# Optimization experiments

Hardware: AMD Instinct MI355X
Metric: run time of the kernel (lower is better)

## Reference

```python
import jax, jax.numpy as jnp
import numpy as np

NEG_SLOPE = 0.3

def capped_lrelu(x):
    # clamp(LeakyReLU_0.3(x), max=1)
    return jnp.minimum(jnp.where(x >= 0, x, NEG_SLOPE * x), 1.0)

def setup_inputs() -> dict:
    key = jax.random.key(0)
    ks = jax.random.split(key, 8)
    B, T, V, H, O = 64, 512, 512, 256, 512
    s = 1.0 / np.sqrt(H)
    return {
        "sentence": jax.random.normal(ks[0], (B, T, V), dtype=jnp.float32),
        "prev_state": jnp.zeros((1, B, H), dtype=jnp.float32),
        "W_ih": jax.random.normal(ks[1], (H, V), dtype=jnp.float32) * s,
        "b_ih": jax.random.normal(ks[2], (H,), dtype=jnp.float32) * s,
        "W_hh": jax.random.normal(ks[3], (H, H), dtype=jnp.float32) * s,
        "b_hh": jax.random.normal(ks[4], (H,), dtype=jnp.float32) * s,
        "W_out": jax.random.normal(ks[5], (O, H), dtype=jnp.float32) * s,
        "b_out": jax.random.normal(ks[6], (O,), dtype=jnp.float32) * s,
    }

def reference(sentence, prev_state, W_ih, b_ih, W_hh, b_hh, W_out, b_out):
    # nn.RNN(nonlinearity='relu'), batch_first, n_layers=1:
    #   h_t = relu(x_t @ W_ih^T + b_ih + h_{t-1} @ W_hh^T + b_hh)
    # Precompute input projections for all timesteps, scan the recurrence.
    x_proj = jnp.einsum('btv,hv->bth', sentence, W_ih) + b_ih  # [B,T,H]
    x_proj_t = jnp.swapaxes(x_proj, 0, 1)                      # [T,B,H]
    h0 = prev_state[0]                                         # [B,H]

    def step(h, xt):
        h_new = jax.nn.relu(xt + h @ W_hh.T + b_hh)
        return h_new, h_new

    h_last, out_seq = jax.lax.scan(step, h0, x_proj_t)         # [T,B,H]
    out_seq = jnp.swapaxes(out_seq, 0, 1)                      # [B,T,H]

    hidden_activ = capped_lrelu(out_seq)
    tags = jax.nn.sigmoid(jnp.einsum('bth,oh->bto', hidden_activ, W_out) + b_out)
    h_n = h_last[None]                                         # [1,B,H]
    return tags, h_n
```

## Files before the change

kernel.cpp:

```cpp
#include <hip/hip_runtime.h>
#include <hip/hip_bf16.h>


typedef __attribute__((ext_vector_type(8))) _Float16 half8;
typedef __attribute__((ext_vector_type(4))) _Float16 half4;
typedef __attribute__((ext_vector_type(4))) float   floatx4;

__device__ __forceinline__ void lds_barrier() {
    asm volatile("s_waitcnt lgkmcnt(0)\n\ts_barrier" ::: "memory");
}

__global__ void conv_weights(const float* __restrict__ wih, const float* __restrict__ wout,
                             _Float16* __restrict__ out) {
    int idx = blockIdx.x * blockDim.x + threadIdx.x;
    const float* src = (idx < 32768) ? wih : wout;
    int j = idx & 32767;
    float4 v = ((const float4*)src)[j];
    half4 h = { (_Float16)v.x, (_Float16)v.y, (_Float16)v.z, (_Float16)v.w };
    ((half4*)out)[idx] = h;
}

__device__ __forceinline__ void stage_weights_swz(const _Float16* __restrict__ src,
                                                  int rowStrideHalves,
                                                  _Float16* lds) {
    int wave = threadIdx.x >> 6;
    int lane = threadIdx.x & 63;
#pragma unroll
    for (int j = 0; j < 16; j++) {
        int Lb = j * 8192 + wave * 1024 + lane * 16;
        int n  = Lb >> 9;
        int c  = Lb & 511;
        int cs = c ^ ((n & 7) << 4);
        const _Float16* g = src + (size_t)n * rowStrideHalves + (cs >> 1);
        _Float16* l = lds + (j * 8192 + wave * 1024) / 2;
        __builtin_amdgcn_global_load_lds((const __attribute__((address_space(1))) void*)g,
                                         (__attribute__((address_space(3))) void*)l,
                                         16, 0, 0);
    }
    asm volatile("s_waitcnt vmcnt(0)" ::: "memory");
    __syncthreads();
}

__global__ __launch_bounds__(512, 2) void gemm1_xproj(const float* __restrict__ A,
                                                      const _Float16* __restrict__ Bw,
                                                      const float* __restrict__ b_ih,
                                                      const float* __restrict__ b_hh,
                                                      float* __restrict__ C) {
    const int K = 512, N = 256;
    __shared__ _Float16 ldsB[65536];
    int wave = threadIdx.x >> 6;
    int lane = threadIdx.x & 63;
    int row  = lane & 15;
    int quad = lane >> 4;
    int m0 = blockIdx.x * 128 + wave * 16;

    floatx4 acc[16];
#pragma unroll
    for (int i = 0; i < 16; i++) acc[i] = (floatx4){0.f, 0.f, 0.f, 0.f};

    const float* pa = A + (size_t)(m0 + row) * K + quad * 8;
    const char* lb = (const char*)ldsB;

    float4 a0s[2], a1s[2];
    a0s[0] = *(const float4*)(pa + 0);   a1s[0] = *(const float4*)(pa + 4);
    a0s[1] = *(const float4*)(pa + 32);  a1s[1] = *(const float4*)(pa + 36);

    for (int h = 0; h < 2; h++) {
        if (h) __syncthreads();
        stage_weights_swz(Bw + h * 256, 512, ldsB);

#pragma unroll
        for (int kk = 0; kk < 256; kk += 32) {
            int kg = h * 256 + kk;
            int s  = (kg >> 5) & 1;
            float4 a0 = a0s[s], a1 = a1s[s];
            if (kg + 64 < 512) {
                a0s[s] = *(const float4*)(pa + kg + 64);
                a1s[s] = *(const float4*)(pa + kg + 68);
            }
            half8 a = { (_Float16)a0.x, (_Float16)a0.y, (_Float16)a0.z, (_Float16)a0.w,
                        (_Float16)a1.x, (_Float16)a1.y, (_Float16)a1.z, (_Float16)a1.w };
#pragma unroll
            for (int nt = 0; nt < 16; nt++) {
                int n = nt * 16 + row;
                int byte = n * 512 + ((quad * 16 + kk * 2) ^ ((n & 7) << 4));
                half8 b = *(const half8*)(lb + byte);
                acc[nt] = __builtin_amdgcn_mfma_f32_16x16x32_f16(a, b, acc[nt], 0, 0, 0);
            }
        }
    }
#pragma unroll
    for (int nt = 0; nt < 16; nt++) {
        int n = nt * 16 + row;
        float bn = b_ih[n] + b_hh[n];
#pragma unroll
        for (int r = 0; r < 4; r++) {
            int m = m0 + quad * 4 + r;
            C[(size_t)m * N + n] = acc[nt][r] + bn;
        }
    }
}

__global__ __launch_bounds__(512, 2) void rnn_recur(const float* __restrict__ xp,
                                                    const float* __restrict__ h0,
                                                    const float* __restrict__ W_hh,
                                                    _Float16* __restrict__ hid,
                                                    float* __restrict__ h_n) {
    const int Hh = 256, T = 512, LD = 264;
    int b0   = blockIdx.x * 16;
    int wave = threadIdx.x >> 6;
    int lane = threadIdx.x & 63;
    int c    = lane & 15;
    int q    = lane >> 4;

    half8 wf[2][8];
#pragma unroll
    for (int nt = 0; nt < 2; nt++) {
        int n = (wave * 2 + nt) * 16 + c;
        const float* wr = W_hh + (size_t)n * Hh + q * 8;
#pragma unroll
        for (int kt = 0; kt < 8; kt++) {
            float4 x0 = *(const float4*)(wr + kt * 32);
            float4 x1 = *(const float4*)(wr + kt * 32 + 4);
            wf[nt][kt] = (half8){ (_Float16)x0.x, (_Float16)x0.y, (_Float16)x0.z, (_Float16)x0.w,
                                  (_Float16)x1.x, (_Float16)x1.y, (_Float16)x1.z, (_Float16)x1.w };
        }
    }

    __shared__ _Float16 hb[2][16][264];
    for (int idx = threadIdx.x; idx < 16 * 256; idx += 512) {
        int m = idx >> 8, k = idx & 255;
        hb[0][m][k] = (_Float16)h0[(size_t)(b0 + m) * Hh + k];
    }
    __syncthreads();

    const float* xpb = xp + (size_t)(b0 + c) * T * Hh;
    _Float16* hidb = hid + (size_t)(b0 + c) * T * Hh;

    int noff[2];
#pragma unroll
    for (int nt = 0; nt < 2; nt++) noff[nt] = (wave * 2 + nt) * 16 + q * 4;

    float4 xq0[2], xq1[2];
#pragma unroll
    for (int nt = 0; nt < 2; nt++) {
        xq0[nt] = *(const float4*)(xpb + (size_t)0 * Hh + noff[nt]);
        xq1[nt] = *(const float4*)(xpb + (size_t)1 * Hh + noff[nt]);
    }
    const float* pf0 = xpb + 2 * Hh;
    const float* pf1 = xpb + 3 * Hh;
    _Float16* hp = hidb;

    auto do_step = [&](int parity, float4 (&xq)[2], const float*& pf,
                       bool prefetch, bool last) {
        const _Float16* hr = &hb[parity][0][0];
        floatx4 aA0 = {0.f,0.f,0.f,0.f}, aA1 = {0.f,0.f,0.f,0.f};
        floatx4 aB0 = {0.f,0.f,0.f,0.f}, aB1 = {0.f,0.f,0.f,0.f};
#pragma unroll
        for (int kt = 0; kt < 4; kt++) {
            half8 hfA = *(const half8*)(hr + c * LD + kt * 32 + q * 8);
            half8 hfB = *(const half8*)(hr + c * LD + (kt + 4) * 32 + q * 8);
            aA0 = __builtin_amdgcn_mfma_f32_16x16x32_f16(wf[0][kt],     hfA, aA0, 0, 0, 0);
            aB0 = __builtin_amdgcn_mfma_f32_16x16x32_f16(wf[0][kt + 4], hfB, aB0, 0, 0, 0);
            aA1 = __builtin_amdgcn_mfma_f32_16x16x32_f16(wf[1][kt],     hfA, aA1, 0, 0, 0);
            aB1 = __builtin_amdgcn_mfma_f32_16x16x32_f16(wf[1][kt + 4], hfB, aB1, 0, 0, 0);
        }
        floatx4 acc[2];
        acc[0] = aA0 + aB0;
        acc[1] = aA1 + aB1;

        _Float16* hw = &hb[parity ^ 1][0][0];
#pragma unroll
        for (int nt = 0; nt < 2; nt++) {
            float v0 = fmaxf(acc[nt][0] + xq[nt].x, 0.f);
            float v1 = fmaxf(acc[nt][1] + xq[nt].y, 0.f);
            float v2 = fmaxf(acc[nt][2] + xq[nt].z, 0.f);
            float v3 = fmaxf(acc[nt][3] + xq[nt].w, 0.f);
            half4 hv = { (_Float16)v0, (_Float16)v1, (_Float16)v2, (_Float16)v3 };
            *(half4*)(hw + c * LD + noff[nt]) = hv;
            *(half4*)(hp + noff[nt]) = hv;
            if (last) {
                float4 hn = { v0, v1, v2, v3 };
                *(float4*)(h_n + (size_t)(b0 + c) * Hh + noff[nt]) = hn;
            }
        }
        hp += Hh;
        if (prefetch) {
#pragma unroll
            for (int nt = 0; nt < 2; nt++)
                xq[nt] = *(const float4*)(pf + noff[nt]);
            pf += 2 * Hh;
        }
        lds_barrier();
    };

    for (int t = 0; t < T - 2; t += 2) {
        do_step(0, xq0, pf0, true, false);
        do_step(1, xq1, pf1, true, false);
    }
    do_step(0, xq0, pf0, false, false);
    do_step(1, xq1, pf1, false, true);
}

__global__ __launch_bounds__(512, 2) void gemm3_tags(const _Float16* __restrict__ A,
                                                     const _Float16* __restrict__ Bw,
                                                     const float* __restrict__ bias,
                                                     float* __restrict__ C) {
    const int K = 256, N = 512;
    __shared__ _Float16 ldsB[65536];
    int wave = threadIdx.x >> 6;
    int lane = threadIdx.x & 63;
    int row  = lane & 15;
    int quad = lane >> 4;
    int m0 = blockIdx.x * 128 + wave * 16;
    int nb = blockIdx.y;

    const _Float16* pa = A + (size_t)(m0 + row) * K + quad * 8;

    half8 as[2];
    as[0] = *(const half8*)(pa + 0);
    as[1] = *(const half8*)(pa + 32);

    stage_weights_swz(Bw + (size_t)nb * 256 * K, K, ldsB);

    floatx4 acc[16];
#pragma unroll
    for (int i = 0; i < 16; i++) acc[i] = (floatx4){0.f, 0.f, 0.f, 0.f};

    const char* lb = (const char*)ldsB;
    const _Float16 one = (_Float16)1.0f;

#pragma unroll
    for (int kk = 0; kk < 256; kk += 32) {
        int s = (kk >> 5) & 1;
        half8 a = as[s];
        if (kk + 64 < 256)
            as[s] = *(const half8*)(pa + kk + 64);
#pragma unroll
        for (int j = 0; j < 8; j++) a[j] = (a[j] < one) ? a[j] : one;
#pragma unroll
        for (int nt = 0; nt < 16; nt++) {
            int n = nt * 16 + row;
            int byte = n * 512 + ((quad * 16 + kk * 2) ^ ((n & 7) << 4));
            half8 b = *(const half8*)(lb + byte);
            acc[nt] = __builtin_amdgcn_mfma_f32_16x16x32_f16(a, b, acc[nt], 0, 0, 0);
        }
    }
#pragma unroll
    for (int nt = 0; nt < 16; nt++) {
        int n = nb * 256 + nt * 16 + row;
        float bn = bias[n];
#pragma unroll
        for (int r = 0; r < 4; r++) {
            int m = m0 + quad * 4 + r;
            float v = acc[nt][r] + bn;
            C[(size_t)m * N + n] = 1.f / (1.f + __expf(-v));
        }
    }
}

extern "C" void kernel_launch(void* const* d_in, const int* in_sizes, int n_in,
                              void* d_out, int out_size, void* d_ws, size_t ws_size,
                              hipStream_t stream) {
    const float* sentence   = (const float*)d_in[0];
    const float* prev_state = (const float*)d_in[1];
    const float* W_ih       = (const float*)d_in[2];
    const float* b_ih       = (const float*)d_in[3];
    const float* W_hh       = (const float*)d_in[4];
    const float* b_hh       = (const float*)d_in[5];
    const float* W_out      = (const float*)d_in[6];
    const float* b_out      = (const float*)d_in[7];

    const size_t WIH_N   = 256u * 512u;
    const size_t WOUT_N  = 512u * 256u;
    const size_t XPROJ_N = 32768u * 256u;
    const size_t HID_N   = 64u * 512u * 256u;

    char* w = (char*)d_ws;
    _Float16* wih_f  = (_Float16*)w;  w += WIH_N * sizeof(_Float16);
    _Float16* wout_f = (_Float16*)w;  w += WOUT_N * sizeof(_Float16);
    float*    xproj  = (float*)w;     w += XPROJ_N * sizeof(float);
    _Float16* hid_f  = (_Float16*)w;  w += HID_N * sizeof(_Float16);

    float* tags = (float*)d_out;
    float* h_n  = (float*)d_out + 16777216;

    conv_weights<<<256, 256, 0, stream>>>(W_ih, W_out, wih_f);

    gemm1_xproj<<<256, 512, 0, stream>>>(sentence, wih_f, b_ih, b_hh, xproj);

    rnn_recur<<<4, 512, 0, stream>>>(xproj, prev_state, W_hh, hid_f, h_n);

    gemm3_tags<<<dim3(256, 2), 512, 0, stream>>>(hid_f, wout_f, b_out, tags);
}
```

Before: 515.8 us.

## Fuse weight conversion into GEMM1 and widen recurrence to 16 waves

```diff
diff --git a/kernel.cpp b/kernel.cpp
--- a/kernel.cpp
+++ b/kernel.cpp
@@ -8,16 +8,6 @@
 
 __device__ __forceinline__ void lds_barrier() {
     asm volatile("s_waitcnt lgkmcnt(0)\n\ts_barrier" ::: "memory");
-}
-
-__global__ void conv_weights(const float* __restrict__ wih, const float* __restrict__ wout,
-                             _Float16* __restrict__ out) {
-    int idx = blockIdx.x * blockDim.x + threadIdx.x;
-    const float* src = (idx < 32768) ? wih : wout;
-    int j = idx & 32767;
-    float4 v = ((const float4*)src)[j];
-    half4 h = { (_Float16)v.x, (_Float16)v.y, (_Float16)v.z, (_Float16)v.w };
-    ((half4*)out)[idx] = h;
 }
 
 __device__ __forceinline__ void stage_weights_swz(const _Float16* __restrict__ src,
@@ -41,11 +31,32 @@
     __syncthreads();
 }
 
+__device__ __forceinline__ void stage_weights_cvt(const float* __restrict__ src,
+                                                  _Float16* lds) {
+    int tid = threadIdx.x;
+#pragma unroll
+    for (int j = 0; j < 16; j++) {
+        int Lb = j * 8192 + tid * 16;
+        int n  = Lb >> 9;
+        int cb = Lb & 511;
+        int k  = (cb ^ ((n & 7) << 4)) >> 1;
+        const float* g = src + (size_t)n * 512 + k;
+        float4 x0 = *(const float4*)(g);
+        float4 x1 = *(const float4*)(g + 4);
+        half8 hv = { (_Float16)x0.x, (_Float16)x0.y, (_Float16)x0.z, (_Float16)x0.w,
+                     (_Float16)x1.x, (_Float16)x1.y, (_Float16)x1.z, (_Float16)x1.w };
+        *(half8*)(lds + Lb / 2) = hv;
+    }
+    __syncthreads();
+}
+
 __global__ __launch_bounds__(512, 2) void gemm1_xproj(const float* __restrict__ A,
-                                                      const _Float16* __restrict__ Bw,
+                                                      const float* __restrict__ Wih32,
+                                                      const float* __restrict__ Wout32,
                                                       const float* __restrict__ b_ih,
                                                       const float* __restrict__ b_hh,
-                                                      float* __restrict__ C) {
+                                                      float* __restrict__ C,
+                                                      _Float16* __restrict__ wout_f) {
     const int K = 512, N = 256;
     __shared__ _Float16 ldsB[65536];
     int wave = threadIdx.x >> 6;
@@ -67,7 +78,7 @@
 
     for (int h = 0; h < 2; h++) {
         if (h) __syncthreads();
-        stage_weights_swz(Bw + h * 256, 512, ldsB);
+        stage_weights_cvt(Wih32 + h * 256, ldsB);
 
 #pragma unroll
         for (int kk = 0; kk < 256; kk += 32) {
@@ -99,13 +110,22 @@
             C[(size_t)m * N + n] = acc[nt][r] + bn;
         }
     }
-}
-
-__global__ __launch_bounds__(512, 2) void rnn_recur(const float* __restrict__ xp,
-                                                    const float* __restrict__ h0,
-                                                    const float* __restrict__ W_hh,
-                                                    _Float16* __restrict__ hid,
-                                                    float* __restrict__ h_n) {
+
+    if (blockIdx.x < 32) {
+        int base = blockIdx.x * 4096 + threadIdx.x * 8;
+        float4 x0 = *(const float4*)(Wout32 + base);
+        float4 x1 = *(const float4*)(Wout32 + base + 4);
+        half8 hv = { (_Float16)x0.x, (_Float16)x0.y, (_Float16)x0.z, (_Float16)x0.w,
+                     (_Float16)x1.x, (_Float16)x1.y, (_Float16)x1.z, (_Float16)x1.w };
+        *(half8*)(wout_f + base) = hv;
+    }
+}
+
+__global__ __launch_bounds__(1024, 4) void rnn_recur(const float* __restrict__ xp,
+                                                     const float* __restrict__ h0,
+                                                     const float* __restrict__ W_hh,
+                                                     _Float16* __restrict__ hid,
+                                                     float* __restrict__ h_n) {
     const int Hh = 256, T = 512, LD = 264;
     int b0   = blockIdx.x * 16;
     int wave = threadIdx.x >> 6;
@@ -113,22 +133,21 @@
     int c    = lane & 15;
     int q    = lane >> 4;
 
-    half8 wf[2][8];
-#pragma unroll
-    for (int nt = 0; nt < 2; nt++) {
-        int n = (wave * 2 + nt) * 16 + c;
+    half8 wf[8];
+    {
+        int n = wave * 16 + c;
         const float* wr = W_hh + (size_t)n * Hh + q * 8;
 #pragma unroll
         for (int kt = 0; kt < 8; kt++) {
             float4 x0 = *(const float4*)(wr + kt * 32);
             float4 x1 = *(const float4*)(wr + kt * 32 + 4);
-            wf[nt][kt] = (half8){ (_Float16)x0.x, (_Float16)x0.y, (_Float16)x0.z, (_Float16)x0.w,
-                                  (_Float16)x1.x, (_Float16)x1.y, (_Float16)x1.z, (_Float16)x1.w };
+            wf[kt] = (half8){ (_Float16)x0.x, (_Float16)x0.y, (_Float16)x0.z, (_Float16)x0.w,
+                              (_Float16)x1.x, (_Float16)x1.y, (_Float16)x1.z, (_Float16)x1.w };
         }
     }
 
     __shared__ _Float16 hb[2][16][264];
-    for (int idx = threadIdx.x; idx < 16 * 256; idx += 512) {
+    for (int idx = threadIdx.x; idx < 16 * 256; idx += 1024) {
         int m = idx >> 8, k = idx & 255;
         hb[0][m][k] = (_Float16)h0[(size_t)(b0 + m) * Hh + k];
     }
@@ -137,58 +156,42 @@
     const float* xpb = xp + (size_t)(b0 + c) * T * Hh;
     _Float16* hidb = hid + (size_t)(b0 + c) * T * Hh;
 
-    int noff[2];
-#pragma unroll
-    for (int nt = 0; nt < 2; nt++) noff[nt] = (wave * 2 + nt) * 16 + q * 4;
-
-    float4 xq0[2], xq1[2];
-#pragma unroll
-    for (int nt = 0; nt < 2; nt++) {
-        xq0[nt] = *(const float4*)(xpb + (size_t)0 * Hh + noff[nt]);
-        xq1[nt] = *(const float4*)(xpb + (size_t)1 * Hh + noff[nt]);
-    }
+    int noff = wave * 16 + q * 4;
+
+    float4 xq0 = *(const float4*)(xpb + (size_t)0 * Hh + noff);
+    float4 xq1 = *(const float4*)(xpb + (size_t)1 * Hh + noff);
     const float* pf0 = xpb + 2 * Hh;
     const float* pf1 = xpb + 3 * Hh;
     _Float16* hp = hidb;
 
-    auto do_step = [&](int parity, float4 (&xq)[2], const float*& pf,
+    auto do_step = [&](int parity, float4& xq, const float*& pf,
                        bool prefetch, bool last) {
         const _Float16* hr = &hb[parity][0][0];
-        floatx4 aA0 = {0.f,0.f,0.f,0.f}, aA1 = {0.f,0.f,0.f,0.f};
-        floatx4 aB0 = {0.f,0.f,0.f,0.f}, aB1 = {0.f,0.f,0.f,0.f};
+        floatx4 aA = {0.f,0.f,0.f,0.f}, aB = {0.f,0.f,0.f,0.f};
 #pragma unroll
         for (int kt = 0; kt < 4; kt++) {
             half8 hfA = *(const half8*)(hr + c * LD + kt * 32 + q * 8);
             half8 hfB = *(const half8*)(hr + c * LD + (kt + 4) * 32 + q * 8);
-            aA0 = __builtin_amdgcn_mfma_f32_16x16x32_f16(wf[0][kt],     hfA, aA0, 0, 0, 0);
-            aB0 = __builtin_amdgcn_mfma_f32_16x16x32_f16(wf[0][kt + 4], hfB, aB0, 0, 0, 0);
-            aA1 = __builtin_amdgcn_mfma_f32_16x16x32_f16(wf[1][kt],     hfA, aA1, 0, 0, 0);
-            aB1 = __builtin_amdgcn_mfma_f32_16x16x32_f16(wf[1][kt + 4], hfB, aB1, 0, 0, 0);
-        }
-        floatx4 acc[2];
-        acc[0] = aA0 + aB0;
-        acc[1] = aA1 + aB1;
+            aA = __builtin_amdgcn_mfma_f32_16x16x32_f16(wf[kt],     hfA, aA, 0, 0, 0);
+            aB = __builtin_amdgcn_mfma_f32_16x16x32_f16(wf[kt + 4], hfB, aB, 0, 0, 0);
+        }
+        floatx4 acc = aA + aB;
 
         _Float16* hw = &hb[parity ^ 1][0][0];
-#pragma unroll
-        for (int nt = 0; nt < 2; nt++) {
-            float v0 = fmaxf(acc[nt][0] + xq[nt].x, 0.f);
-            float v1 = fmaxf(acc[nt][1] + xq[nt].y, 0.f);
-            float v2 = fmaxf(acc[nt][2] + xq[nt].z, 0.f);
-            float v3 = fmaxf(acc[nt][3] + xq[nt].w, 0.f);
-            half4 hv = { (_Float16)v0, (_Float16)v1, (_Float16)v2, (_Float16)v3 };
-            *(half4*)(hw + c * LD + noff[nt]) = hv;
-            *(half4*)(hp + noff[nt]) = hv;
-            if (last) {
-                float4 hn = { v0, v1, v2, v3 };
-                *(float4*)(h_n + (size_t)(b0 + c) * Hh + noff[nt]) = hn;
-            }
+        float v0 = fmaxf(acc[0] + xq.x, 0.f);
+        float v1 = fmaxf(acc[1] + xq.y, 0.f);
+        float v2 = fmaxf(acc[2] + xq.z, 0.f);
+        float v3 = fmaxf(acc[3] + xq.w, 0.f);
+        half4 hv = { (_Float16)v0, (_Float16)v1, (_Float16)v2, (_Float16)v3 };
+        *(half4*)(hw + c * LD + noff) = hv;
+        *(half4*)(hp + noff) = hv;
+        if (last) {
+            float4 hn = { v0, v1, v2, v3 };
+            *(float4*)(h_n + (size_t)(b0 + c) * Hh + noff) = hn;
         }
         hp += Hh;
         if (prefetch) {
-#pragma unroll
-            for (int nt = 0; nt < 2; nt++)
-                xq[nt] = *(const float4*)(pf + noff[nt]);
+            xq = *(const float4*)(pf + noff);
             pf += 2 * Hh;
         }
         lds_barrier();
@@ -271,13 +274,11 @@
     const float* W_out      = (const float*)d_in[6];
     const float* b_out      = (const float*)d_in[7];
 
-    const size_t WIH_N   = 256u * 512u;
     const size_t WOUT_N  = 512u * 256u;
     const size_t XPROJ_N = 32768u * 256u;
     const size_t HID_N   = 64u * 512u * 256u;
 
     char* w = (char*)d_ws;
-    _Float16* wih_f  = (_Float16*)w;  w += WIH_N * sizeof(_Float16);
     _Float16* wout_f = (_Float16*)w;  w += WOUT_N * sizeof(_Float16);
     float*    xproj  = (float*)w;     w += XPROJ_N * sizeof(float);
     _Float16* hid_f  = (_Float16*)w;  w += HID_N * sizeof(_Float16);
@@ -285,11 +286,9 @@
     float* tags = (float*)d_out;
     float* h_n  = (float*)d_out + 16777216;
 
-    conv_weights<<<256, 256, 0, stream>>>(W_ih, W_out, wih_f);
-
-    gemm1_xproj<<<256, 512, 0, stream>>>(sentence, wih_f, b_ih, b_hh, xproj);
-
-    rnn_recur<<<4, 512, 0, stream>>>(xproj, prev_state, W_hh, hid_f, h_n);
+    gemm1_xproj<<<256, 512, 0, stream>>>(sentence, W_ih, W_out, b_ih, b_hh, xproj, wout_f);
+
+    rnn_recur<<<4, 1024, 0, stream>>>(xproj, prev_state, W_hh, hid_f, h_n);
 
     gemm3_tags<<<dim3(256, 2), 512, 0, stream>>>(hid_f, wout_f, b_out, tags);
 }
```

After: 560.7 us. 1.09x slower.
